# Performance work log

Measured on AMD Instinct MI355X. Metric: run time of the kernel, lower is better.

The kernel has to match this reference:

```python
import jax, jax.numpy as jnp
import numpy as np

WS = (7, 7)          # window size
SS = (3, 3)          # shift size
NUM_HEADS = 6


def _relative_position_index(ws):
    ch, cw = np.meshgrid(np.arange(ws[0]), np.arange(ws[1]), indexing='ij')
    coords = np.stack([ch, cw]).reshape(2, -1)           # [2, N]
    rel = coords[:, :, None] - coords[:, None, :]        # [2, N, N]
    rel = rel.transpose(1, 2, 0)
    rel[:, :, 0] += ws[0] - 1
    rel[:, :, 1] += ws[1] - 1
    rel[:, :, 0] *= 2 * ws[1] - 1
    return rel.sum(-1).reshape(-1)                       # [N*N]


def _shift_mask(pad_H, pad_W, ws, ss):
    # per-window additive mask [num_windows, N, N], -100 across shift regions
    img = np.zeros((pad_H, pad_W))
    h_slices = ((0, -ws[0]), (-ws[0], -ss[0]), (-ss[0], None))
    w_slices = ((0, -ws[1]), (-ws[1], -ss[1]), (-ss[1], None))
    cnt = 0
    for h in h_slices:
        for w in w_slices:
            img[h[0]:h[1], w[0]:w[1]] = cnt
            cnt += 1
    m = img.reshape(pad_H // ws[0], ws[0], pad_W // ws[1], ws[1])
    m = m.transpose(0, 2, 1, 3).reshape(-1, ws[0] * ws[1])   # [nW, N]
    diff = m[:, None, :] - m[:, :, None]
    return np.where(diff != 0, -100.0, 0.0).astype(np.float32)


def setup_inputs() -> dict:
    key = jax.random.key(0)
    ks = jax.random.split(key, 6)
    B, H, W, C = 16, 112, 112, 192
    return {
        'x': jax.random.normal(ks[0], (B, H, W, C), jnp.float32),
        'qkv_w': jax.random.normal(ks[1], (3 * C, C), jnp.float32) * (C ** -0.5),
        'qkv_b': jax.random.normal(ks[2], (3 * C,), jnp.float32) * 0.02,
        'proj_w': jax.random.normal(ks[3], (C, C), jnp.float32) * (C ** -0.5),
        'proj_b': jax.random.normal(ks[4], (C,), jnp.float32) * 0.02,
        'rel_bias_table': jax.random.normal(ks[5], ((2 * WS[0] - 1) * (2 * WS[1] - 1), NUM_HEADS), jnp.float32) * 0.02,
    }


def reference(x, qkv_w, qkv_b, proj_w, proj_b, rel_bias_table):
    B, H, W, C = x.shape
    ws, ss = WS, SS
    N = ws[0] * ws[1]
    hd = C // NUM_HEADS

    pad_r = (ws[1] - W % ws[1]) % ws[1]
    pad_b = (ws[0] - H % ws[0]) % ws[0]
    x = jnp.pad(x, ((0, 0), (0, pad_b), (0, pad_r), (0, 0)))
    pad_H, pad_W = H + pad_b, W + pad_r
    ss = (0 if ws[0] >= pad_H else ss[0], 0 if ws[1] >= pad_W else ss[1])
    shifted = sum(ss) > 0

    if shifted:
        x = jnp.roll(x, (-ss[0], -ss[1]), axis=(1, 2))

    nWh, nWw = pad_H // ws[0], pad_W // ws[1]
    nW = nWh * nWw
    # window partition -> [B*nW, N, C]
    x = x.reshape(B, nWh, ws[0], nWw, ws[1], C).transpose(0, 1, 3, 2, 4, 5).reshape(B * nW, N, C)

    qkv = x @ qkv_w.T + qkv_b                               # [B*nW, N, 3C]
    qkv = qkv.reshape(B * nW, N, 3, NUM_HEADS, hd).transpose(2, 0, 3, 1, 4)
    q, k, v = qkv[0], qkv[1], qkv[2]                        # [B*nW, h, N, hd]

    q = q * (hd ** -0.5)
    attn = jnp.einsum('whnd,whmd->whnm', q, k)              # [B*nW, h, N, N]

    rel_idx = _relative_position_index(ws)
    rel_bias = rel_bias_table[rel_idx].reshape(N, N, NUM_HEADS).transpose(2, 0, 1)
    attn = attn + rel_bias[None]

    if shifted:
        mask = jnp.asarray(_shift_mask(pad_H, pad_W, ws, ss))   # [nW, N, N]
        attn = attn.reshape(B, nW, NUM_HEADS, N, N) + mask[None, :, None]
        attn = attn.reshape(B * nW, NUM_HEADS, N, N)

    attn = jax.nn.softmax(attn, axis=-1)
    out = jnp.einsum('whnm,whmd->whnd', attn, v)            # [B*nW, h, N, hd]
    out = out.transpose(0, 2, 1, 3).reshape(B * nW, N, C)
    out = out @ proj_w.T + proj_b

    out = out.reshape(B, nWh, nWw, ws[0], ws[1], C).transpose(0, 1, 3, 2, 4, 5).reshape(B, pad_H, pad_W, C)
    if shifted:
        out = jnp.roll(out, (ss[0], ss[1]), axis=(1, 2))
    return out[:, :H, :W, :]
```

## Files before the change

kernel.cpp:

```cpp
#include <hip/hip_runtime.h>

typedef __bf16 bf16_t;
typedef __bf16 bf16x8 __attribute__((ext_vector_type(8)));
typedef __bf16 bf16x4 __attribute__((ext_vector_type(4)));
typedef float  f32x4  __attribute__((ext_vector_type(4)));

#define MFMA16(a,b,c) __builtin_amdgcn_mfma_f32_16x16x32_bf16((a),(b),(c),0,0,0)

#define REG_STRIDE 200
#define VT_STRIDE  68
#define REG_ELEMS  13056
#define SC_STRIDE  40
#define SC_CHUNK   640
#define BT_OFF     (REG_ELEMS + 6 * SC_CHUNK)
#define SMEM_ELEMS (BT_OFF + 1014)
#define FSTRIDE    196

#define WPROJ_OFF 110592

__global__ void convert_w_kernel(const float* __restrict__ qkv_w,
                                 const float* __restrict__ proj_w,
                                 bf16_t* __restrict__ wb) {
    const int i = (blockIdx.x * 256 + threadIdx.x) * 4;
    float4 f;
    if (i < WPROJ_OFF) f = *(const float4*)(qkv_w + i);
    else               f = *(const float4*)(proj_w + (i - WPROJ_OFF));
    bf16x4 v;
    v[0] = (bf16_t)f.x; v[1] = (bf16_t)f.y; v[2] = (bf16_t)f.z; v[3] = (bf16_t)f.w;
    *(bf16x4*)(wb + i) = v;
}

__device__ __forceinline__ void gemm64x32(const bf16_t* __restrict__ xa,
                                          const bf16_t* __restrict__ w0,
                                          const bf16_t* __restrict__ w1,
                                          f32x4 acc[4][2]) {
    bf16x8 b0 = *(const bf16x8*)(w0);
    bf16x8 b1 = *(const bf16x8*)(w1);
    bf16x8 n0 = *(const bf16x8*)(w0 + 32);
    bf16x8 n1 = *(const bf16x8*)(w1 + 32);
    #pragma unroll
    for (int ks = 0; ks < 6; ++ks) {
        bf16x8 m0, m1;
        if (ks < 4) {
            m0 = *(const bf16x8*)(w0 + (ks + 2) * 32);
            m1 = *(const bf16x8*)(w1 + (ks + 2) * 32);
        }
        #pragma unroll
        for (int mi = 0; mi < 4; ++mi) {
            const bf16x8 afr = *(const bf16x8*)(xa + (mi * 16) * REG_STRIDE + ks * 32);
            acc[mi][0] = MFMA16(afr, b0, acc[mi][0]);
            acc[mi][1] = MFMA16(afr, b1, acc[mi][1]);
        }
        b0 = n0; b1 = n1; n0 = m0; n1 = m1;
    }
}

__global__ __launch_bounds__(384, 5)
void swin_fused_kernel(const float* __restrict__ x,
                       const bf16_t* __restrict__ wbuf,
                       const float* __restrict__ qkv_b,
                       const float* __restrict__ proj_b,
                       const float* __restrict__ tbl,
                       float* __restrict__ out)
{
    __shared__ __align__(16) bf16_t smem[SMEM_ELEMS];
    bf16_t* region = smem;
    bf16_t* bt     = smem + BT_OFF;

    const int tid    = threadIdx.x;
    const int lane   = tid & 63;
    const int wave   = tid >> 6;
    const int lanelo = lane & 15;
    const int quad   = lane >> 4;

    bf16_t* sc = smem + REG_ELEMS + wave * SC_CHUNK;

    const int blk = blockIdx.x;
    const int b   = blk >> 8;
    const int wh  = (blk >> 4) & 15;
    const int ww  = blk & 15;
    const int rowbase = wh * 7 + 3;
    const int colbase = ww * 7 + 3;

    for (int i = tid; i < 1014; i += 384) bt[i] = (bf16_t)tbl[i];

    for (int idx = tid; idx < 64 * 48; idx += 384) {
        const int t  = idx / 48;
        const int c4 = (idx - t * 48) * 4;
        bf16x4 v4;
        if (t < 49) {
            int gr = rowbase + t / 7;  if (gr >= 112) gr -= 112;
            int gc = colbase + t % 7;  if (gc >= 112) gc -= 112;
            const float4 f = *(const float4*)(x + (((long)b * 112 + gr) * 112 + gc) * 192 + c4);
            v4[0] = (bf16_t)f.x; v4[1] = (bf16_t)f.y;
            v4[2] = (bf16_t)f.z; v4[3] = (bf16_t)f.w;
        } else {
            v4[0] = (bf16_t)0.0f; v4[1] = (bf16_t)0.0f;
            v4[2] = (bf16_t)0.0f; v4[3] = (bf16_t)0.0f;
        }
        *(bf16x4*)(region + t * REG_STRIDE + c4) = v4;
    }
    __syncthreads();

    const int h = wave;
    const bf16_t* xa = region + lanelo * REG_STRIDE + quad * 8;

    bf16x8 qa[4], kb[4];
    f32x4  vacc[4][2];
    {
        {
            const bf16_t* wb = wbuf + (0 * 192 + h * 32) * 192;
            f32x4 acc[4][2] = {};
            gemm64x32(xa, wb + lanelo * 192 + quad * 8, wb + (16 + lanelo) * 192 + quad * 8, acc);
            const float bias0 = qkv_b[0 * 192 + h * 32 + lanelo];
            const float bias1 = qkv_b[0 * 192 + h * 32 + 16 + lanelo];
            #pragma unroll
            for (int mi = 0; mi < 4; ++mi) {
                #pragma unroll
                for (int r = 0; r < 4; ++r) {
                    sc[(quad * 4 + r) * SC_STRIDE + lanelo]      = (bf16_t)(acc[mi][0][r] + bias0);
                    sc[(quad * 4 + r) * SC_STRIDE + 16 + lanelo] = (bf16_t)(acc[mi][1][r] + bias1);
                }
                qa[mi] = *(const bf16x8*)(sc + lanelo * SC_STRIDE + quad * 8);
            }
        }
        {
            const bf16_t* wb = wbuf + (1 * 192 + h * 32) * 192;
            f32x4 acc[4][2] = {};
            gemm64x32(xa, wb + lanelo * 192 + quad * 8, wb + (16 + lanelo) * 192 + quad * 8, acc);
            const float bias0 = qkv_b[1 * 192 + h * 32 + lanelo];
            const float bias1 = qkv_b[1 * 192 + h * 32 + 16 + lanelo];
            #pragma unroll
            for (int mi = 0; mi < 4; ++mi) {
                #pragma unroll
                for (int r = 0; r < 4; ++r) {
                    sc[(quad * 4 + r) * SC_STRIDE + lanelo]      = (bf16_t)(acc[mi][0][r] + bias0);
                    sc[(quad * 4 + r) * SC_STRIDE + 16 + lanelo] = (bf16_t)(acc[mi][1][r] + bias1);
                }
                kb[mi] = *(const bf16x8*)(sc + lanelo * SC_STRIDE + quad * 8);
            }
        }
        {
            const bf16_t* wb = wbuf + (2 * 192 + h * 32) * 192;
            f32x4 acc[4][2] = {};
            gemm64x32(xa, wb + lanelo * 192 + quad * 8, wb + (16 + lanelo) * 192 + quad * 8, acc);
            #pragma unroll
            for (int mi = 0; mi < 4; ++mi) {
                vacc[mi][0] = acc[mi][0];
                vacc[mi][1] = acc[mi][1];
            }
        }
    }
    __syncthreads();

    {
        const float bias0 = qkv_b[2 * 192 + h * 32 + lanelo];
        const float bias1 = qkv_b[2 * 192 + h * 32 + 16 + lanelo];
        #pragma unroll
        for (int mi = 0; mi < 4; ++mi)
            #pragma unroll
            for (int r = 0; r < 4; ++r) {
                const int tok = quad * 4 + r + 16 * mi;
                region[(h * 32 + lanelo) * VT_STRIDE + tok]      = (bf16_t)(vacc[mi][0][r] + bias0);
                region[(h * 32 + 16 + lanelo) * VT_STRIDE + tok] = (bf16_t)(vacc[mi][1][r] + bias1);
            }
    }

    f32x4 o_[4][2] = {};
    {
        const float scale = 0.17677669529663687f;

        int kvalid[4], kch[4], kcw[4], kid[4];
        #pragma unroll
        for (int ni = 0; ni < 4; ++ni) {
            const int col = ni * 16 + lanelo;
            kvalid[ni] = (col < 49);
            const int cc = kvalid[ni] ? col : 48;
            kch[ni] = cc / 7; kcw[ni] = cc - kch[ni] * 7;
            const int gr = wh * 7 + kch[ni], gc = ww * 7 + kcw[ni];
            kid[ni] = (gr < 105 ? 0 : (gr < 109 ? 1 : 2)) * 3 + (gc < 105 ? 0 : (gc < 109 ? 1 : 2));
        }

        const bf16x8 bv00 = *(const bf16x8*)(region + (h * 32 + lanelo) * VT_STRIDE + quad * 8);
        const bf16x8 bv01 = *(const bf16x8*)(region + (h * 32 + 16 + lanelo) * VT_STRIDE + quad * 8);
        const bf16x8 bv10 = *(const bf16x8*)(region + (h * 32 + lanelo) * VT_STRIDE + 32 + quad * 8);
        const bf16x8 bv11 = *(const bf16x8*)(region + (h * 32 + 16 + lanelo) * VT_STRIDE + 32 + quad * 8);

        #pragma unroll
        for (int mi = 0; mi < 4; ++mi) {
            f32x4 s[4];
            #pragma unroll
            for (int ni = 0; ni < 4; ++ni) {
                f32x4 z = {0.f, 0.f, 0.f, 0.f};
                s[ni] = MFMA16(qa[mi], kb[ni], z);
            }
            #pragma unroll
            for (int r = 0; r < 4; ++r) {
                const int row = mi * 16 + quad * 4 + r;
                const int rq  = (row < 49) ? row : 48;
                const int rh  = rq / 7, rw = rq - (rq / 7) * 7;
                const int gqr = wh * 7 + rh, gqc = ww * 7 + rw;
                const int idq = (gqr < 105 ? 0 : (gqr < 109 ? 1 : 2)) * 3 + (gqc < 105 ? 0 : (gqc < 109 ? 1 : 2));
                #pragma unroll
                for (int ni = 0; ni < 4; ++ni) {
                    float v;
                    if (kvalid[ni]) {
                        const int bidx = ((rh - kch[ni] + 6) * 13 + (rw - kcw[ni] + 6)) * 6 + h;
                        v = s[ni][r] * scale + (float)bt[bidx];
                        if (idq != kid[ni]) v -= 100.0f;
                    } else {
                        v = -1e30f;
                    }
                    s[ni][r] = v;
                }
                float m0 = fmaxf(fmaxf(s[0][r], s[1][r]), fmaxf(s[2][r], s[3][r]));
                m0 = fmaxf(m0, __shfl_xor(m0, 1));
                m0 = fmaxf(m0, __shfl_xor(m0, 2));
                m0 = fmaxf(m0, __shfl_xor(m0, 4));
                m0 = fmaxf(m0, __shfl_xor(m0, 8));
                float sum = 0.f;
                #pragma unroll
                for (int ni = 0; ni < 4; ++ni) {
                    const float e = __expf(s[ni][r] - m0);
                    s[ni][r] = e;
                    sum += e;
                }
                sum += __shfl_xor(sum, 1);
                sum += __shfl_xor(sum, 2);
                sum += __shfl_xor(sum, 4);
                sum += __shfl_xor(sum, 8);
                const float rinv = 1.0f / sum;
                sc[(quad * 4 + r) * SC_STRIDE + lanelo]      = (bf16_t)(s[0][r] * rinv);
                sc[(quad * 4 + r) * SC_STRIDE + 16 + lanelo] = (bf16_t)(s[1][r] * rinv);
                s[2][r] *= rinv;
                s[3][r] *= rinv;
            }
            {
                const bf16x8 ap = *(const bf16x8*)(sc + lanelo * SC_STRIDE + quad * 8);
                o_[mi][0] = MFMA16(ap, bv00, o_[mi][0]);
                o_[mi][1] = MFMA16(ap, bv01, o_[mi][1]);
            }
            #pragma unroll
            for (int r = 0; r < 4; ++r) {
                sc[(quad * 4 + r) * SC_STRIDE + lanelo]      = (bf16_t)s[2][r];
                sc[(quad * 4 + r) * SC_STRIDE + 16 + lanelo] = (bf16_t)s[3][r];
            }
            {
                const bf16x8 ap = *(const bf16x8*)(sc + lanelo * SC_STRIDE + quad * 8);
                o_[mi][0] = MFMA16(ap, bv10, o_[mi][0]);
                o_[mi][1] = MFMA16(ap, bv11, o_[mi][1]);
            }
        }
    }
    __syncthreads();

    #pragma unroll
    for (int mi = 0; mi < 4; ++mi)
        #pragma unroll
        for (int r = 0; r < 4; ++r) {
            const int row = quad * 4 + r + 16 * mi;
            region[row * REG_STRIDE + h * 32 + lanelo]      = (bf16_t)(o_[mi][0][r]);
            region[row * REG_STRIDE + h * 32 + 16 + lanelo] = (bf16_t)(o_[mi][1][r]);
        }
    __syncthreads();

    {
        const bf16_t* wb = wbuf + WPROJ_OFF + (wave * 32) * 192;
        f32x4 acc[4][2] = {};
        gemm64x32(xa, wb + lanelo * 192 + quad * 8, wb + (16 + lanelo) * 192 + quad * 8, acc);
        const int o0 = wave * 32 + lanelo;
        const float pb0 = proj_b[o0];
        const float pb1 = proj_b[o0 + 16];
        float* freg = (float*)smem;
        __syncthreads();
        #pragma unroll
        for (int half = 0; half < 2; ++half) {
            #pragma unroll
            for (int mi = 0; mi < 2; ++mi) {
                const int ami = half * 2 + mi;
                #pragma unroll
                for (int r = 0; r < 4; ++r) {
                    const int row = quad * 4 + r + 16 * mi;
                    freg[row * FSTRIDE + o0]      = acc[ami][0][r] + pb0;
                    freg[row * FSTRIDE + o0 + 16] = acc[ami][1][r] + pb1;
                }
            }
            __syncthreads();
            const int lim = half ? 816 : 1536;
            for (int idx = tid; idx < lim; idx += 384) {
                const int t  = idx / 48;
                const int cc = (idx - t * 48) * 4;
                const int tok = half * 32 + t;
                int gr = rowbase + tok / 7;  if (gr >= 112) gr -= 112;
                int gc = colbase + tok % 7;  if (gc >= 112) gc -= 112;
                const float4 v = *(const float4*)(freg + t * FSTRIDE + cc);
                *(float4*)(out + (((long)b * 112 + gr) * 112 + gc) * 192 + cc) = v;
            }
            if (!half) __syncthreads();
        }
    }
}

extern "C" void kernel_launch(void* const* d_in, const int* in_sizes, int n_in,
                              void* d_out, int out_size, void* d_ws, size_t ws_size,
                              hipStream_t stream) {
    const float* x      = (const float*)d_in[0];
    const float* qkv_w  = (const float*)d_in[1];
    const float* qkv_b  = (const float*)d_in[2];
    const float* proj_w = (const float*)d_in[3];
    const float* proj_b = (const float*)d_in[4];
    const float* tbl    = (const float*)d_in[5];
    bf16_t* wbuf = (bf16_t*)d_ws;

    convert_w_kernel<<<144, 256, 0, stream>>>(qkv_w, proj_w, wbuf);
    swin_fused_kernel<<<4096, 384, 0, stream>>>(x, wbuf, qkv_b, proj_b, tbl,
                                                (float*)d_out);
}
```

Baseline: 533.6 us.

## Transpose score MFMA, swizzle scratch LDS, add setprio and nontemporal I/O

Computes scores as K·Qᵀ so each lane owns one query row. The softmax reductions then need only two cross-quad shuffles instead of per-row four-step shuffles. The per-wave scratch becomes a 64-column XOR-swizzled buffer so the full probability row is written once and read as two fragments, and mask and bias index data are precomputed and packed per key. It also adds s_setprio around MFMA groups, raises the launch-bounds occupancy hint from 5 to 6, unrolls the input load, and uses nontemporal loads and stores for x and out. The larger scratch and the higher occupancy target raise LDS use and register pressure, which risks spills.

Result: slower. 640.6 us (+20.0%).

```diff
diff --git a/kernel.cpp b/kernel.cpp
--- a/kernel.cpp
+++ b/kernel.cpp
@@ -10,9 +10,9 @@
 #define REG_STRIDE 200
 #define VT_STRIDE  68
 #define REG_ELEMS  13056
-#define SC_STRIDE  40
-#define SC_CHUNK   640
-#define BT_OFF     (REG_ELEMS + 6 * SC_CHUNK)
+#define SC_CHUNK   1024
+#define SC_OFF     REG_ELEMS
+#define BT_OFF     (SC_OFF + 6 * SC_CHUNK)
 #define SMEM_ELEMS (BT_OFF + 1014)
 #define FSTRIDE    196
 
@@ -28,6 +28,11 @@
     bf16x4 v;
     v[0] = (bf16_t)f.x; v[1] = (bf16_t)f.y; v[2] = (bf16_t)f.z; v[3] = (bf16_t)f.w;
     *(bf16x4*)(wb + i) = v;
+}
+
+__device__ __forceinline__ bf16_t* scp(bf16_t* sc, int row, int col) {
+    const int byte = (row * 128 + col * 2) ^ ((row & 7) << 4);
+    return (bf16_t*)((char*)sc + byte);
 }
 
 __device__ __forceinline__ void gemm64x32(const bf16_t* __restrict__ xa,
@@ -45,17 +50,33 @@
             m0 = *(const bf16x8*)(w0 + (ks + 2) * 32);
             m1 = *(const bf16x8*)(w1 + (ks + 2) * 32);
         }
+        __builtin_amdgcn_s_setprio(1);
         #pragma unroll
         for (int mi = 0; mi < 4; ++mi) {
             const bf16x8 afr = *(const bf16x8*)(xa + (mi * 16) * REG_STRIDE + ks * 32);
             acc[mi][0] = MFMA16(afr, b0, acc[mi][0]);
             acc[mi][1] = MFMA16(afr, b1, acc[mi][1]);
         }
+        __builtin_amdgcn_s_setprio(0);
         b0 = n0; b1 = n1; n0 = m0; n1 = m1;
     }
 }
 
-__global__ __launch_bounds__(384, 5)
+__device__ __forceinline__ void roundtrip(bf16_t* __restrict__ sc, int lanelo, int quad,
+                                          const f32x4 acc[4][2], float bias0, float bias1,
+                                          bf16x8 outfr[4]) {
+    #pragma unroll
+    for (int mi = 0; mi < 4; ++mi) {
+        #pragma unroll
+        for (int r = 0; r < 4; ++r) {
+            *scp(sc, quad * 4 + r, lanelo)      = (bf16_t)(acc[mi][0][r] + bias0);
+            *scp(sc, quad * 4 + r, 16 + lanelo) = (bf16_t)(acc[mi][1][r] + bias1);
+        }
+        outfr[mi] = *(const bf16x8*)scp(sc, lanelo, quad * 8);
+    }
+}
+
+__global__ __launch_bounds__(384, 6)
 void swin_fused_kernel(const float* __restrict__ x,
                        const bf16_t* __restrict__ wbuf,
                        const float* __restrict__ qkv_b,
@@ -73,7 +94,7 @@
     const int lanelo = lane & 15;
     const int quad   = lane >> 4;
 
-    bf16_t* sc = smem + REG_ELEMS + wave * SC_CHUNK;
+    bf16_t* sc = smem + SC_OFF + wave * SC_CHUNK;
 
     const int blk = blockIdx.x;
     const int b   = blk >> 8;
@@ -84,21 +105,27 @@
 
     for (int i = tid; i < 1014; i += 384) bt[i] = (bf16_t)tbl[i];
 
-    for (int idx = tid; idx < 64 * 48; idx += 384) {
-        const int t  = idx / 48;
-        const int c4 = (idx - t * 48) * 4;
-        bf16x4 v4;
-        if (t < 49) {
-            int gr = rowbase + t / 7;  if (gr >= 112) gr -= 112;
-            int gc = colbase + t % 7;  if (gc >= 112) gc -= 112;
-            const float4 f = *(const float4*)(x + (((long)b * 112 + gr) * 112 + gc) * 192 + c4);
-            v4[0] = (bf16_t)f.x; v4[1] = (bf16_t)f.y;
-            v4[2] = (bf16_t)f.z; v4[3] = (bf16_t)f.w;
-        } else {
-            v4[0] = (bf16_t)0.0f; v4[1] = (bf16_t)0.0f;
-            v4[2] = (bf16_t)0.0f; v4[3] = (bf16_t)0.0f;
-        }
-        *(bf16x4*)(region + t * REG_STRIDE + c4) = v4;
+    {
+        const int t0  = tid / 48;
+        const int c0  = tid - t0 * 48;
+        const int cb4 = c0 * 4;
+        #pragma unroll
+        for (int it = 0; it < 8; ++it) {
+            const int t = t0 + it * 8;
+            bf16x4 v4;
+            if (t < 49) {
+                int gr = rowbase + t / 7;  if (gr >= 112) gr -= 112;
+                int gc = colbase + t % 7;  if (gc >= 112) gc -= 112;
+                const f32x4 f = __builtin_nontemporal_load(
+                    (const f32x4*)(x + (((long)b * 112 + gr) * 112 + gc) * 192 + cb4));
+                v4[0] = (bf16_t)f[0]; v4[1] = (bf16_t)f[1];
+                v4[2] = (bf16_t)f[2]; v4[3] = (bf16_t)f[3];
+            } else {
+                v4[0] = (bf16_t)0.0f; v4[1] = (bf16_t)0.0f;
+                v4[2] = (bf16_t)0.0f; v4[3] = (bf16_t)0.0f;
+            }
+            *(bf16x4*)(region + t * REG_STRIDE + cb4) = v4;
+        }
     }
     __syncthreads();
 
@@ -112,33 +139,15 @@
             const bf16_t* wb = wbuf + (0 * 192 + h * 32) * 192;
             f32x4 acc[4][2] = {};
             gemm64x32(xa, wb + lanelo * 192 + quad * 8, wb + (16 + lanelo) * 192 + quad * 8, acc);
-            const float bias0 = qkv_b[0 * 192 + h * 32 + lanelo];
-            const float bias1 = qkv_b[0 * 192 + h * 32 + 16 + lanelo];
-            #pragma unroll
-            for (int mi = 0; mi < 4; ++mi) {
-                #pragma unroll
-                for (int r = 0; r < 4; ++r) {
-                    sc[(quad * 4 + r) * SC_STRIDE + lanelo]      = (bf16_t)(acc[mi][0][r] + bias0);
-                    sc[(quad * 4 + r) * SC_STRIDE + 16 + lanelo] = (bf16_t)(acc[mi][1][r] + bias1);
-                }
-                qa[mi] = *(const bf16x8*)(sc + lanelo * SC_STRIDE + quad * 8);
-            }
+            roundtrip(sc, lanelo, quad, acc,
+                      qkv_b[0 * 192 + h * 32 + lanelo], qkv_b[0 * 192 + h * 32 + 16 + lanelo], qa);
         }
         {
             const bf16_t* wb = wbuf + (1 * 192 + h * 32) * 192;
             f32x4 acc[4][2] = {};
             gemm64x32(xa, wb + lanelo * 192 + quad * 8, wb + (16 + lanelo) * 192 + quad * 8, acc);
-            const float bias0 = qkv_b[1 * 192 + h * 32 + lanelo];
-            const float bias1 = qkv_b[1 * 192 + h * 32 + 16 + lanelo];
-            #pragma unroll
-            for (int mi = 0; mi < 4; ++mi) {
-                #pragma unroll
-                for (int r = 0; r < 4; ++r) {
-                    sc[(quad * 4 + r) * SC_STRIDE + lanelo]      = (bf16_t)(acc[mi][0][r] + bias0);
-                    sc[(quad * 4 + r) * SC_STRIDE + 16 + lanelo] = (bf16_t)(acc[mi][1][r] + bias1);
-                }
-                kb[mi] = *(const bf16x8*)(sc + lanelo * SC_STRIDE + quad * 8);
-            }
+            roundtrip(sc, lanelo, quad, acc,
+                      qkv_b[1 * 192 + h * 32 + lanelo], qkv_b[1 * 192 + h * 32 + 16 + lanelo], kb);
         }
         {
             const bf16_t* wb = wbuf + (2 * 192 + h * 32) * 192;
@@ -170,16 +179,18 @@
     {
         const float scale = 0.17677669529663687f;
 
-        int kvalid[4], kch[4], kcw[4], kid[4];
-        #pragma unroll
-        for (int ni = 0; ni < 4; ++ni) {
-            const int col = ni * 16 + lanelo;
-            kvalid[ni] = (col < 49);
-            const int cc = kvalid[ni] ? col : 48;
-            kch[ni] = cc / 7; kcw[ni] = cc - kch[ni] * 7;
-            const int gr = wh * 7 + kch[ni], gc = ww * 7 + kcw[ni];
-            kid[ni] = (gr < 105 ? 0 : (gr < 109 ? 1 : 2)) * 3 + (gc < 105 ? 0 : (gc < 109 ? 1 : 2));
-        }
+        int kp[4][4];
+        #pragma unroll
+        for (int ni = 0; ni < 4; ++ni)
+            #pragma unroll
+            for (int r = 0; r < 4; ++r) {
+                const int k  = ni * 16 + quad * 4 + r;
+                const int kk = (k < 49) ? k : 48;
+                const int kh = kk / 7, kw = kk - kh * 7;
+                const int gr = wh * 7 + kh, gc = ww * 7 + kw;
+                const int kid = (gr < 105 ? 0 : (gr < 109 ? 1 : 2)) * 3 + (gc < 105 ? 0 : (gc < 109 ? 1 : 2));
+                kp[ni][r] = (((6 - kh) * 13 + (6 - kw)) * 6) | (kid << 12) | ((k < 49) << 16);
+            }
 
         const bf16x8 bv00 = *(const bf16x8*)(region + (h * 32 + lanelo) * VT_STRIDE + quad * 8);
         const bf16x8 bv01 = *(const bf16x8*)(region + (h * 32 + 16 + lanelo) * VT_STRIDE + quad * 8);
@@ -188,67 +199,65 @@
 
         #pragma unroll
         for (int mi = 0; mi < 4; ++mi) {
-            f32x4 s[4];
+            f32x4 st[4];
+            __builtin_amdgcn_s_setprio(1);
             #pragma unroll
             for (int ni = 0; ni < 4; ++ni) {
                 f32x4 z = {0.f, 0.f, 0.f, 0.f};
-                s[ni] = MFMA16(qa[mi], kb[ni], z);
-            }
-            #pragma unroll
-            for (int r = 0; r < 4; ++r) {
-                const int row = mi * 16 + quad * 4 + r;
-                const int rq  = (row < 49) ? row : 48;
-                const int rh  = rq / 7, rw = rq - (rq / 7) * 7;
-                const int gqr = wh * 7 + rh, gqc = ww * 7 + rw;
-                const int idq = (gqr < 105 ? 0 : (gqr < 109 ? 1 : 2)) * 3 + (gqc < 105 ? 0 : (gqc < 109 ? 1 : 2));
+                st[ni] = MFMA16(kb[ni], qa[mi], z);
+            }
+            __builtin_amdgcn_s_setprio(0);
+
+            const int q   = mi * 16 + lanelo;
+            const int qq  = (q < 49) ? q : 48;
+            const int qh  = qq / 7, qw = qq - qh * 7;
+            const int gqr = wh * 7 + qh, gqc = ww * 7 + qw;
+            const int qid = (gqr < 105 ? 0 : (gqr < 109 ? 1 : 2)) * 3 + (gqc < 105 ? 0 : (gqc < 109 ? 1 : 2));
+            const int qoff = (qh * 13 + qw) * 6 + h;
+
+            float sv[4][4];
+            float m0 = -1e30f;
+            #pragma unroll
+            for (int ni = 0; ni < 4; ++ni)
                 #pragma unroll
-                for (int ni = 0; ni < 4; ++ni) {
-                    float v;
-                    if (kvalid[ni]) {
-                        const int bidx = ((rh - kch[ni] + 6) * 13 + (rw - kcw[ni] + 6)) * 6 + h;
-                        v = s[ni][r] * scale + (float)bt[bidx];
-                        if (idq != kid[ni]) v -= 100.0f;
-                    } else {
-                        v = -1e30f;
-                    }
-                    s[ni][r] = v;
+                for (int r = 0; r < 4; ++r) {
+                    const int p = kp[ni][r];
+                    float v = st[ni][r] * scale + (float)bt[qoff + (p & 0xfff)];
+                    if (qid != ((p >> 12) & 0xf)) v -= 100.0f;
+                    if (!(p >> 16)) v = -1e30f;
+                    sv[ni][r] = v;
+                    m0 = fmaxf(m0, v);
                 }
-                float m0 = fmaxf(fmaxf(s[0][r], s[1][r]), fmaxf(s[2][r], s[3][r]));
-                m0 = fmaxf(m0, __shfl_xor(m0, 1));
-                m0 = fmaxf(m0, __shfl_xor(m0, 2));
-                m0 = fmaxf(m0, __shfl_xor(m0, 4));
-                m0 = fmaxf(m0, __shfl_xor(m0, 8));
-                float sum = 0.f;
+            m0 = fmaxf(m0, __shfl_xor(m0, 16));
+            m0 = fmaxf(m0, __shfl_xor(m0, 32));
+            float sum = 0.f;
+            #pragma unroll
+            for (int ni = 0; ni < 4; ++ni)
                 #pragma unroll
-                for (int ni = 0; ni < 4; ++ni) {
-                    const float e = __expf(s[ni][r] - m0);
-                    s[ni][r] = e;
+                for (int r = 0; r < 4; ++r) {
+                    const float e = __expf(sv[ni][r] - m0);
+                    sv[ni][r] = e;
                     sum += e;
                 }
-                sum += __shfl_xor(sum, 1);
-                sum += __shfl_xor(sum, 2);
-                sum += __shfl_xor(sum, 4);
-                sum += __shfl_xor(sum, 8);
-                const float rinv = 1.0f / sum;
-                sc[(quad * 4 + r) * SC_STRIDE + lanelo]      = (bf16_t)(s[0][r] * rinv);
-                sc[(quad * 4 + r) * SC_STRIDE + 16 + lanelo] = (bf16_t)(s[1][r] * rinv);
-                s[2][r] *= rinv;
-                s[3][r] *= rinv;
-            }
+            sum += __shfl_xor(sum, 16);
+            sum += __shfl_xor(sum, 32);
+            const float rinv = 1.0f / sum;
+
+            #pragma unroll
+            for (int ni = 0; ni < 4; ++ni)
+                #pragma unroll
+                for (int r = 0; r < 4; ++r)
+                    *scp(sc, lanelo, ni * 16 + quad * 4 + r) = (bf16_t)(sv[ni][r] * rinv);
+
             {
-                const bf16x8 ap = *(const bf16x8*)(sc + lanelo * SC_STRIDE + quad * 8);
-                o_[mi][0] = MFMA16(ap, bv00, o_[mi][0]);
-                o_[mi][1] = MFMA16(ap, bv01, o_[mi][1]);
-            }
-            #pragma unroll
-            for (int r = 0; r < 4; ++r) {
-                sc[(quad * 4 + r) * SC_STRIDE + lanelo]      = (bf16_t)s[2][r];
-                sc[(quad * 4 + r) * SC_STRIDE + 16 + lanelo] = (bf16_t)s[3][r];
-            }
-            {
-                const bf16x8 ap = *(const bf16x8*)(sc + lanelo * SC_STRIDE + quad * 8);
-                o_[mi][0] = MFMA16(ap, bv10, o_[mi][0]);
-                o_[mi][1] = MFMA16(ap, bv11, o_[mi][1]);
+                const bf16x8 ap0 = *(const bf16x8*)scp(sc, lanelo, quad * 8);
+                const bf16x8 ap1 = *(const bf16x8*)scp(sc, lanelo, 32 + quad * 8);
+                __builtin_amdgcn_s_setprio(1);
+                o_[mi][0] = MFMA16(ap0, bv00, o_[mi][0]);
+                o_[mi][1] = MFMA16(ap0, bv01, o_[mi][1]);
+                o_[mi][0] = MFMA16(ap1, bv10, o_[mi][0]);
+                o_[mi][1] = MFMA16(ap1, bv11, o_[mi][1]);
+                __builtin_amdgcn_s_setprio(0);
             }
         }
     }
@@ -293,8 +302,9 @@
                 const int tok = half * 32 + t;
                 int gr = rowbase + tok / 7;  if (gr >= 112) gr -= 112;
                 int gc = colbase + tok % 7;  if (gc >= 112) gc -= 112;
-                const float4 v = *(const float4*)(freg + t * FSTRIDE + cc);
-                *(float4*)(out + (((long)b * 112 + gr) * 112 + gc) * 192 + cc) = v;
+                const f32x4 v = *(const f32x4*)(freg + t * FSTRIDE + cc);
+                __builtin_nontemporal_store(v,
+                    (f32x4*)(out + (((long)b * 112 + gr) * 112 + gc) * 192 + cc));
             }
             if (!half) __syncthreads();
         }
```
